# Performance work log

Hardware: AMD Instinct MI355X
Metric: run time of the kernel (lower is better)

Reference implementation:

```python
import jax, jax.numpy as jnp
import numpy as np

ALPHA = 0.01  # ELU slope from init kwargs


def setup_inputs() -> dict:
    key = jax.random.key(0)
    k1, k2, k3, k4, k5 = jax.random.split(key, 5)
    B, L, D_IN, D_ATT = 8, 2048, 256, 128
    context = jax.random.normal(k1, (B, L, D_IN), dtype=jnp.float32)
    query = jax.random.normal(k2, (B, L, D_IN), dtype=jnp.float32)
    query_mask = jax.random.randint(k3, (B, L), 0, 2, dtype=jnp.int32)
    # Linear(in_size, attention_size, bias=False) weights (stored as [in, out])
    W_in = jax.random.normal(k4, (D_IN, D_ATT), dtype=jnp.float32) * 0.05
    W_mem = jax.random.normal(k5, (D_IN, D_ATT), dtype=jnp.float32) * 0.05
    return {"context": context, "query": query, "W_in": W_in,
            "W_mem": W_mem, "query_mask": query_mask}


def reference(context, query, W_in, W_mem, query_mask):
    # VariationalDropout is identity at inference; Linear -> ELU(alpha=0.01)
    inp = jax.nn.elu(jnp.einsum('bld,df->blf', context, W_in), ALPHA)   # [B, Lc, Datt]
    mem = jax.nn.elu(jnp.einsum('bld,df->blf', query, W_mem), ALPHA)    # [B, Lq, Datt]
    scale = inp.shape[-1] ** 0.5
    logits = jnp.einsum('bcf,bqf->bcq', inp, mem) / scale               # [B, Lc, Lq]
    big = jnp.finfo(logits.dtype).max
    # mask_diag=True: kill diagonal (self) positions
    Lq = logits.shape[-1]
    eye = jnp.eye(Lq, dtype=bool)
    logits = jnp.where(eye[None, :, :], -big, logits)
    # masked_softmax over the query axis using query_mask [B, Lq]
    valid = (query_mask > 0)[:, None, :]                                # [B, 1, Lq]
    logits = jnp.where(valid, logits, -big)
    score = jax.nn.softmax(logits, axis=-1)                             # [B, Lc, Lq]
    return jnp.einsum('bcq,bqd->bcd', score, query)                     # [B, Lc, D_in]
```

## Files before the change

### kernel.cpp

```cpp
#include <hip/hip_runtime.h>
#include <math.h>

typedef short v4s __attribute__((ext_vector_type(4)));
typedef short v8s __attribute__((ext_vector_type(8)));
typedef float v4f __attribute__((ext_vector_type(4)));

#define L2E 1.4426950408889634f
#define INV_SCALE 0.08838834764831845f
#define SCL2 (INV_SCALE * L2E)

static __device__ __forceinline__ short f2bf(float x) {
    union { float f; unsigned u; } c; c.f = x;
    unsigned u = c.u;
    unsigned r = (u + 0x7fffu + ((u >> 16) & 1u)) >> 16;
    return (short)r;
}

typedef __attribute__((address_space(3))) void lds_vt;
typedef __attribute__((address_space(1))) const void gl_vt;
static __device__ __forceinline__ void gload_lds16(const void* g, void* l) {
    __builtin_amdgcn_global_load_lds((gl_vt*)g, (lds_vt*)l, 16, 0, 0);
}

__global__ __launch_bounds__(256) void k_pre(const float* __restrict__ ctx,
                                             const float* __restrict__ qry,
                                             const float* __restrict__ Win,
                                             const float* __restrict__ Wmem,
                                             const int* __restrict__ qmask,
                                             short* __restrict__ Qa,
                                             short* __restrict__ Ka,
                                             short* __restrict__ VaT,
                                             float* __restrict__ maskadd) {
    __shared__ __align__(16) char sbuf[64 * 264 * 2];
    int x = blockIdx.x;
    int tid = threadIdx.x;
    if (x < 1024) {
        short* WtS = (short*)sbuf;
        int msel = x & 255, isel = (x >> 8) & 1, nh = (x >> 9) & 1;
        const float* X = isel ? qry : ctx;
        const float* W = isel ? Wmem : Win;
        short* Y = isel ? Ka : Qa;
#pragma unroll 8
        for (int i = 0; i < 64; ++i) {
            int id = i * 256 + tid;
            int k = id >> 6, fp = id & 63;
            WtS[fp * 264 + k] = f2bf(W[k * 128 + nh * 64 + fp]);
        }
        __syncthreads();

        int w = tid >> 6, lane = tid & 63;
        int ln = lane & 15, qd = lane >> 4;
        int m0 = msel * 64 + w * 16;
        v4f zero = {0.f, 0.f, 0.f, 0.f};
        v4f o[4];
#pragma unroll
        for (int i = 0; i < 4; ++i) o[i] = zero;
#pragma unroll
        for (int kk = 0; kk < 8; ++kk) {
            const float* xp = X + (size_t)(m0 + ln) * 256 + kk * 32 + qd * 8;
            float4 x0 = *(const float4*)xp;
            float4 x1 = *(const float4*)(xp + 4);
            v8s a;
            a[0] = f2bf(x0.x); a[1] = f2bf(x0.y); a[2] = f2bf(x0.z); a[3] = f2bf(x0.w);
            a[4] = f2bf(x1.x); a[5] = f2bf(x1.y); a[6] = f2bf(x1.z); a[7] = f2bf(x1.w);
#pragma unroll
            for (int nt = 0; nt < 4; ++nt) {
                v8s bfr = *(const v8s*)(WtS + (nt * 16 + ln) * 264 + kk * 32 + qd * 8);
                o[nt] = __builtin_amdgcn_mfma_f32_16x16x32_bf16(a, bfr, o[nt], 0, 0, 0);
            }
        }
#pragma unroll
        for (int nt = 0; nt < 4; ++nt) {
#pragma unroll
            for (int r = 0; r < 4; ++r) {
                float v = o[nt][r];
                v = v > 0.f ? v : 0.01f * (__expf(v) - 1.f);
                Y[(size_t)(m0 + qd * 4 + r) * 128 + (nh * 4 + nt) * 16 + ln] = f2bf(v);
            }
        }
    } else {
        float (*tile)[65] = (float(*)[65])sbuf;
        int t = x - 1024;
        int q0 = (t & 31) * 64, d0 = ((t >> 5) & 3) * 64, b = t >> 7;
        int c = tid & 63;
        int r4 = tid >> 6;
#pragma unroll
        for (int i = 0; i < 16; ++i) {
            int r = r4 + i * 4;
            tile[r][c] = qry[(size_t)(b * 2048 + q0 + r) * 256 + d0 + c];
        }
        __syncthreads();
        int g = c >> 3, j = c & 7;
#pragma unroll
        for (int i = 0; i < 16; ++i) {
            int d = r4 + i * 4;
            int cs = ((g ^ (d & 7)) << 3) | j;
            VaT[(size_t)(b * 256 + d0 + d) * 2048 + q0 + cs] = f2bf(tile[c][d]);
        }
        if (d0 == 0 && tid < 64) {
            int qq = b * 2048 + q0 + tid;
            maskadd[qq] = (qmask[qq] > 0) ? 0.f : -__builtin_inff();
        }
    }
}

template<int NSPLIT, bool DIRECT>
__global__ __launch_bounds__(256, 2) void k_attn(const short* __restrict__ Qa,
                                                 const short* __restrict__ Ka,
                                                 const short* __restrict__ VaT,
                                                 const float* __restrict__ maskadd,
                                                 float* __restrict__ Opart,
                                                 float* __restrict__ lpart,
                                                 float* __restrict__ out) {
    __shared__ __align__(16) short VaS[2][256 * 64];
    __shared__ __align__(16) short PS[64 * 72];
    __shared__ float lS[4 * 64];

    const int STEPS = 32 / NSPLIT;
    int blk = blockIdx.x;
    int b = blk & 7;
    int t = blk >> 3;
    int c0 = (t & 31) * 64;
    int sp = t >> 5;
    int kv0 = sp * (2048 / NSPLIT);

    int tid = threadIdx.x;
    int w = tid >> 6, lane = tid & 63, ln = lane & 15, qd = lane >> 4;

    const short* qbase = Qa + (size_t)(b * 2048) * 128;
    const short* kbase = Ka + (size_t)(b * 2048 + kv0 + w * 16 + ln) * 128 + qd * 8;
    const short* vbase = VaT + (size_t)(b * 256) * 2048;
    const float* mbase = maskadd + b * 2048 + kv0 + w * 16 + qd * 4;

    v8s qf[4][4];
#pragma unroll
    for (int ct = 0; ct < 4; ++ct) {
        const short* qp = qbase + (size_t)(c0 + ct * 16 + ln) * 128 + qd * 8;
#pragma unroll
        for (int kk = 0; kk < 4; ++kk) qf[ct][kk] = *(const v8s*)(qp + kk * 32);
    }

    v4f zero = {0.f, 0.f, 0.f, 0.f};
    v4f o[4][4];
#pragma unroll
    for (int i = 0; i < 4; ++i)
#pragma unroll
        for (int j = 0; j < 4; ++j) o[i][j] = zero;
    float lacc[4] = {0.f, 0.f, 0.f, 0.f};

    auto stageV = [&](int q0s, int buf) {
        short* base = &VaS[buf][0] + w * 4096;
#pragma unroll
        for (int j = 0; j < 8; ++j) {
            int U = (w * 8 + j) * 64 + lane;
            int d = U >> 3, cc = U & 7;
            gload_lds16(vbase + (size_t)d * 2048 + q0s + cc * 8,
                        base + j * 512);
        }
    };

    stageV(kv0, 0);

    for (int it = 0; it < STEPS; ++it) {
        int q0 = kv0 + it * 64;
        int pb = it & 1;
        stageV(kv0 + ((it + 1) & (STEPS - 1)) * 64, pb ^ 1);

        v8s kf[4];
        const short* kp = kbase + (size_t)it * (64 * 128);
#pragma unroll
        for (int kk = 0; kk < 4; ++kk) kf[kk] = *(const v8s*)(kp + kk * 32);

        float4 mk = *(const float4*)(mbase + it * 64);
        int kvb = q0 + w * 16 + qd * 4;
#pragma unroll
        for (int ct = 0; ct < 4; ++ct) {
            v4f s = zero;
#pragma unroll
            for (int kk = 0; kk < 4; ++kk)
                s = __builtin_amdgcn_mfma_f32_16x16x32_bf16(kf[kk], qf[ct][kk], s, 0, 0, 0);
            int cg = c0 + ct * 16 + ln;
            v4s pw;
            float ls = 0.f;
#pragma unroll
            for (int r = 0; r < 4; ++r) {
                float v = s[r] * SCL2 + (&mk.x)[r];
                if (kvb + r == cg) v = -__builtin_inff();
                float p = exp2f(v);
                ls += p;
                pw[r] = f2bf(p);
            }
            lacc[ct] += ls;
            *(v4s*)(PS + (ct * 16 + ln) * 72 + w * 16 + qd * 4) = pw;
        }
        __syncthreads();

        const short* vs = &VaS[pb][0];
#pragma unroll
        for (int kk2 = 0; kk2 < 2; ++kk2) {
            v8s pf[4], vf[4];
#pragma unroll
            for (int ct = 0; ct < 4; ++ct)
                pf[ct] = *(const v8s*)(PS + (ct * 16 + ln) * 72 + kk2 * 32 + qd * 8);
#pragma unroll
            for (int dt = 0; dt < 4; ++dt) {
                int d = w * 64 + dt * 16 + ln;
                vf[dt] = *(const v8s*)(vs + d * 64 + (((kk2 * 4 + qd) ^ (ln & 7)) << 3));
            }
#pragma unroll
            for (int ct = 0; ct < 4; ++ct)
#pragma unroll
                for (int dt = 0; dt < 4; ++dt)
                    o[ct][dt] = __builtin_amdgcn_mfma_f32_16x16x32_bf16(pf[ct], vf[dt], o[ct][dt], 0, 0, 0);
        }
        __syncthreads();
    }

#pragma unroll
    for (int ct = 0; ct < 4; ++ct) {
        float v = lacc[ct];
        v += __shfl_xor(v, 16);
        v += __shfl_xor(v, 32);
        if (qd == 0) lS[w * 64 + ct * 16 + ln] = v;
    }
    __syncthreads();

#pragma unroll
    for (int ct = 0; ct < 4; ++ct) {
        float4 l0 = *(const float4*)(lS + 0 * 64 + ct * 16 + qd * 4);
        float4 l1 = *(const float4*)(lS + 1 * 64 + ct * 16 + qd * 4);
        float4 l2 = *(const float4*)(lS + 2 * 64 + ct * 16 + qd * 4);
        float4 l3 = *(const float4*)(lS + 3 * 64 + ct * 16 + qd * 4);
        float lv[4];
#pragma unroll
        for (int r = 0; r < 4; ++r)
            lv[r] = (&l0.x)[r] + (&l1.x)[r] + (&l2.x)[r] + (&l3.x)[r];
        int rowg = b * 2048 + c0 + ct * 16 + qd * 4;
        if (DIRECT) {
#pragma unroll
            for (int r = 0; r < 4; ++r) {
                float inv = 1.f / lv[r];
#pragma unroll
                for (int dt = 0; dt < 4; ++dt)
                    out[(size_t)(rowg + r) * 256 + w * 64 + dt * 16 + ln] = o[ct][dt][r] * inv;
            }
        } else {
            float* op = Opart + (size_t)sp * (16384 * 256);
#pragma unroll
            for (int r = 0; r < 4; ++r)
#pragma unroll
                for (int dt = 0; dt < 4; ++dt)
                    op[(size_t)(rowg + r) * 256 + w * 64 + dt * 16 + ln] = o[ct][dt][r];
            if (ln == 0)
                *(float4*)(lpart + sp * 16384 + rowg) = make_float4(lv[0], lv[1], lv[2], lv[3]);
        }
    }
}

template<int NSPLIT>
__global__ __launch_bounds__(256) void k_combine(const float* __restrict__ Opart,
                                                 const float* __restrict__ lpart,
                                                 float* __restrict__ out) {
    int idx = blockIdx.x * 256 + threadIdx.x;
    int row = idx >> 6, d4 = (idx & 63) * 4;
    float L = 0.f;
    float4 acc = {0.f, 0.f, 0.f, 0.f};
#pragma unroll
    for (int s = 0; s < NSPLIT; ++s) {
        L += lpart[s * 16384 + row];
        float4 v = *(const float4*)(Opart + (size_t)s * (16384 * 256) + (size_t)row * 256 + d4);
        acc.x += v.x; acc.y += v.y; acc.z += v.z; acc.w += v.w;
    }
    float inv = 1.f / L;
    float4 res = {acc.x * inv, acc.y * inv, acc.z * inv, acc.w * inv};
    *(float4*)(out + (size_t)row * 256 + d4) = res;
}

extern "C" void kernel_launch(void* const* d_in, const int* in_sizes, int n_in,
                              void* d_out, int out_size, void* d_ws, size_t ws_size,
                              hipStream_t stream) {
    const float* ctx  = (const float*)d_in[0];
    const float* qry  = (const float*)d_in[1];
    const float* win  = (const float*)d_in[2];
    const float* wmem = (const float*)d_in[3];
    const int* qmask  = (const int*)d_in[4];
    float* out = (float*)d_out;

    char* ws = (char*)d_ws;
    short* Qa      = (short*)(ws);
    short* Ka      = (short*)(ws + (4u << 20));
    short* VaT     = (short*)(ws + (8u << 20));
    float* maskadd = (float*)(ws + (16u << 20));
    float* lpart   = (float*)(ws + (16u << 20) + 131072);
    float* Opart   = (float*)(ws + (18u << 20));

    k_pre<<<dim3(2048), 256, 0, stream>>>(ctx, qry, win, wmem, qmask,
                                          Qa, Ka, VaT, maskadd);

    const size_t base = 18u << 20, part = 16u << 20;
    if (ws_size >= base + 2 * part) {
        k_attn<2, false><<<dim3(512), 256, 0, stream>>>(Qa, Ka, VaT, maskadd, Opart, lpart, out);
        k_combine<2><<<dim3(4096), 256, 0, stream>>>(Opart, lpart, out);
    } else {
        k_attn<1, true><<<dim3(256), 256, 0, stream>>>(Qa, Ka, VaT, maskadd, Opart, lpart, out);
    }
}
```

Before: 147.7 us.

## Replace KV split-and-combine with 32-row context tiles and software-pipelined attention loop

The attention kernel no longer splits the key range in two with a separate combine kernel. It now uses 512 blocks of 32 context rows, each covering the full key range and writing normalized output directly. The loop is unrolled by two with double-buffered K/mask register prefetch, a double-buffered swizzled P tile in LDS, manual waitcnt/barrier instead of two __syncthreads, and raised priority around the PV MFMAs. This removes the partial-output round trip through global memory and the extra launch. In exchange, each block reads all of V and K for half as many rows, doubling K/V traffic per output row. The hand-set vmcnt value is fragile if the load count changes.

```diff
diff --git a/kernel.cpp b/kernel.cpp
--- a/kernel.cpp
+++ b/kernel.cpp
@@ -104,49 +104,42 @@
     }
 }
 
-template<int NSPLIT, bool DIRECT>
 __global__ __launch_bounds__(256, 2) void k_attn(const short* __restrict__ Qa,
                                                  const short* __restrict__ Ka,
                                                  const short* __restrict__ VaT,
                                                  const float* __restrict__ maskadd,
-                                                 float* __restrict__ Opart,
-                                                 float* __restrict__ lpart,
                                                  float* __restrict__ out) {
     __shared__ __align__(16) short VaS[2][256 * 64];
-    __shared__ __align__(16) short PS[64 * 72];
-    __shared__ float lS[4 * 64];
-
-    const int STEPS = 32 / NSPLIT;
+    __shared__ __align__(16) short PSb[2][32 * 64];
+
+    const int STEPS = 32;
     int blk = blockIdx.x;
     int b = blk & 7;
-    int t = blk >> 3;
-    int c0 = (t & 31) * 64;
-    int sp = t >> 5;
-    int kv0 = sp * (2048 / NSPLIT);
+    int c0 = (blk >> 3) * 32;
 
     int tid = threadIdx.x;
     int w = tid >> 6, lane = tid & 63, ln = lane & 15, qd = lane >> 4;
 
     const short* qbase = Qa + (size_t)(b * 2048) * 128;
-    const short* kbase = Ka + (size_t)(b * 2048 + kv0 + w * 16 + ln) * 128 + qd * 8;
+    const short* kbase = Ka + (size_t)(b * 2048 + w * 16 + ln) * 128 + qd * 8;
     const short* vbase = VaT + (size_t)(b * 256) * 2048;
-    const float* mbase = maskadd + b * 2048 + kv0 + w * 16 + qd * 4;
-
-    v8s qf[4][4];
-#pragma unroll
-    for (int ct = 0; ct < 4; ++ct) {
+    const float* mbase = maskadd + b * 2048 + w * 16 + qd * 4;
+
+    v8s qf[2][4];
+#pragma unroll
+    for (int ct = 0; ct < 2; ++ct) {
         const short* qp = qbase + (size_t)(c0 + ct * 16 + ln) * 128 + qd * 8;
 #pragma unroll
         for (int kk = 0; kk < 4; ++kk) qf[ct][kk] = *(const v8s*)(qp + kk * 32);
     }
 
     v4f zero = {0.f, 0.f, 0.f, 0.f};
-    v4f o[4][4];
-#pragma unroll
-    for (int i = 0; i < 4; ++i)
+    v4f o[2][4];
+#pragma unroll
+    for (int i = 0; i < 2; ++i)
 #pragma unroll
         for (int j = 0; j < 4; ++j) o[i][j] = zero;
-    float lacc[4] = {0.f, 0.f, 0.f, 0.f};
+    float lacc[2] = {0.f, 0.f};
 
     auto stageV = [&](int q0s, int buf) {
         short* base = &VaS[buf][0] + w * 4096;
@@ -159,121 +152,113 @@
         }
     };
 
-    stageV(kv0, 0);
-
-    for (int it = 0; it < STEPS; ++it) {
-        int q0 = kv0 + it * 64;
-        int pb = it & 1;
-        stageV(kv0 + ((it + 1) & (STEPS - 1)) * 64, pb ^ 1);
-
-        v8s kf[4];
-        const short* kp = kbase + (size_t)it * (64 * 128);
-#pragma unroll
-        for (int kk = 0; kk < 4; ++kk) kf[kk] = *(const v8s*)(kp + kk * 32);
-
-        float4 mk = *(const float4*)(mbase + it * 64);
-        int kvb = q0 + w * 16 + qd * 4;
-#pragma unroll
-        for (int ct = 0; ct < 4; ++ct) {
-            v4f s = zero;
-#pragma unroll
-            for (int kk = 0; kk < 4; ++kk)
-                s = __builtin_amdgcn_mfma_f32_16x16x32_bf16(kf[kk], qf[ct][kk], s, 0, 0, 0);
-            int cg = c0 + ct * 16 + ln;
-            v4s pw;
-            float ls = 0.f;
-#pragma unroll
-            for (int r = 0; r < 4; ++r) {
-                float v = s[r] * SCL2 + (&mk.x)[r];
-                if (kvb + r == cg) v = -__builtin_inff();
-                float p = exp2f(v);
-                ls += p;
-                pw[r] = f2bf(p);
-            }
-            lacc[ct] += ls;
-            *(v4s*)(PS + (ct * 16 + ln) * 72 + w * 16 + qd * 4) = pw;
-        }
-        __syncthreads();
-
-        const short* vs = &VaS[pb][0];
-#pragma unroll
-        for (int kk2 = 0; kk2 < 2; ++kk2) {
-            v8s pf[4], vf[4];
-#pragma unroll
-            for (int ct = 0; ct < 4; ++ct)
-                pf[ct] = *(const v8s*)(PS + (ct * 16 + ln) * 72 + kk2 * 32 + qd * 8);
-#pragma unroll
-            for (int dt = 0; dt < 4; ++dt) {
-                int d = w * 64 + dt * 16 + ln;
-                vf[dt] = *(const v8s*)(vs + d * 64 + (((kk2 * 4 + qd) ^ (ln & 7)) << 3));
-            }
-#pragma unroll
-            for (int ct = 0; ct < 4; ++ct)
-#pragma unroll
-                for (int dt = 0; dt < 4; ++dt)
-                    o[ct][dt] = __builtin_amdgcn_mfma_f32_16x16x32_bf16(pf[ct], vf[dt], o[ct][dt], 0, 0, 0);
-        }
-        __syncthreads();
-    }
-
-#pragma unroll
-    for (int ct = 0; ct < 4; ++ct) {
+    stageV(0, 0);
+    v8s kfA[4], kfB[4];
+    float4 mkA, mkB;
+#pragma unroll
+    for (int kk = 0; kk < 4; ++kk) kfA[kk] = *(const v8s*)(kbase + kk * 32);
+    mkA = *(const float4*)(mbase);
+
+#define ATT_STEP(IT, KFC, MKC, KFN, MKN) do {                                  \
+    int q0 = (IT) * 64;                                                        \
+    int pb = (IT) & 1;                                                         \
+    int itn = ((IT) + 1) & (STEPS - 1);                                        \
+    stageV(itn * 64, pb ^ 1);                                                  \
+    {                                                                          \
+        const short* kp = kbase + (size_t)itn * 8192;                          \
+        _Pragma("unroll")                                                      \
+        for (int kk = 0; kk < 4; ++kk) KFN[kk] = *(const v8s*)(kp + kk * 32);  \
+        MKN = *(const float4*)(mbase + itn * 64);                              \
+    }                                                                          \
+      \
+    asm volatile("s_waitcnt vmcnt(13)" ::: "memory");                          \
+    short* PScur = &PSb[pb][0];                                                \
+    int kvb = q0 + w * 16 + qd * 4;                                            \
+    _Pragma("unroll")                                                          \
+    for (int ct = 0; ct < 2; ++ct) {                                           \
+        v4f s = zero;                                                          \
+        _Pragma("unroll")                                                      \
+        for (int kk = 0; kk < 4; ++kk)                                         \
+            s = __builtin_amdgcn_mfma_f32_16x16x32_bf16(KFC[kk], qf[ct][kk],   \
+                                                        s, 0, 0, 0);           \
+        int cg = c0 + ct * 16 + ln;                                            \
+        v4s pw;                                                                \
+        float ls = 0.f;                                                        \
+        _Pragma("unroll")                                                      \
+        for (int r = 0; r < 4; ++r) {                                          \
+            float v = s[r] * SCL2 + (&MKC.x)[r];                               \
+            if (kvb + r == cg) v = -__builtin_inff();                          \
+            float p = exp2f(v);                                                \
+            ls += p;                                                           \
+            pw[r] = f2bf(p);                                                   \
+        }                                                                      \
+        lacc[ct] += ls;                                                        \
+        int hs = ((w * 2 + (qd >> 1)) ^ (ln & 7));                             \
+        *(v4s*)(PScur + (ct * 16 + ln) * 64 + hs * 8 + (qd & 1) * 4) = pw;     \
+    }                                                                          \
+    asm volatile("s_waitcnt lgkmcnt(0)" ::: "memory");                         \
+    __builtin_amdgcn_s_barrier();                                              \
+    asm volatile("" ::: "memory");                                             \
+    const short* vs = &VaS[pb][0];                                             \
+    __builtin_amdgcn_s_setprio(1);                                             \
+    _Pragma("unroll")                                                          \
+    for (int kk2 = 0; kk2 < 2; ++kk2) {                                        \
+        v8s pf[2], vf[4];                                                      \
+        _Pragma("unroll")                                                      \
+        for (int ct = 0; ct < 2; ++ct)                                         \
+            pf[ct] = *(const v8s*)(PScur + (ct * 16 + ln) * 64 +               \
+                                   (((kk2 * 4 + qd) ^ (ln & 7)) << 3));        \
+        _Pragma("unroll")                                                      \
+        for (int dt = 0; dt < 4; ++dt) {                                       \
+            int d = w * 64 + dt * 16 + ln;                                     \
+            vf[dt] = *(const v8s*)(vs + d * 64 +                               \
+                                   (((kk2 * 4 + qd) ^ (ln & 7)) << 3));        \
+        }                                                                      \
+        _Pragma("unroll")                                                      \
+        for (int ct = 0; ct < 2; ++ct)                                         \
+            _Pragma("unroll")                                                  \
+            for (int dt = 0; dt < 4; ++dt)                                     \
+                o[ct][dt] = __builtin_amdgcn_mfma_f32_16x16x32_bf16(           \
+                    pf[ct], vf[dt], o[ct][dt], 0, 0, 0);                       \
+    }                                                                          \
+    __builtin_amdgcn_s_setprio(0);                                             \
+} while (0)
+
+#pragma unroll 1
+    for (int it2 = 0; it2 < STEPS; it2 += 2) {
+        ATT_STEP(it2, kfA, mkA, kfB, mkB);
+        ATT_STEP(it2 + 1, kfB, mkB, kfA, mkA);
+    }
+#undef ATT_STEP
+
+    __syncthreads();
+    float* lS = (float*)&PSb[0][0];
+#pragma unroll
+    for (int ct = 0; ct < 2; ++ct) {
         float v = lacc[ct];
         v += __shfl_xor(v, 16);
         v += __shfl_xor(v, 32);
-        if (qd == 0) lS[w * 64 + ct * 16 + ln] = v;
+        if (qd == 0) lS[w * 32 + ct * 16 + ln] = v;
     }
     __syncthreads();
 
 #pragma unroll
-    for (int ct = 0; ct < 4; ++ct) {
-        float4 l0 = *(const float4*)(lS + 0 * 64 + ct * 16 + qd * 4);
-        float4 l1 = *(const float4*)(lS + 1 * 64 + ct * 16 + qd * 4);
-        float4 l2 = *(const float4*)(lS + 2 * 64 + ct * 16 + qd * 4);
-        float4 l3 = *(const float4*)(lS + 3 * 64 + ct * 16 + qd * 4);
-        float lv[4];
-#pragma unroll
-        for (int r = 0; r < 4; ++r)
-            lv[r] = (&l0.x)[r] + (&l1.x)[r] + (&l2.x)[r] + (&l3.x)[r];
+    for (int ct = 0; ct < 2; ++ct) {
+        float4 l0 = *(const float4*)(lS + 0 * 32 + ct * 16 + qd * 4);
+        float4 l1 = *(const float4*)(lS + 1 * 32 + ct * 16 + qd * 4);
+        float4 l2 = *(const float4*)(lS + 2 * 32 + ct * 16 + qd * 4);
+        float4 l3 = *(const float4*)(lS + 3 * 32 + ct * 16 + qd * 4);
         int rowg = b * 2048 + c0 + ct * 16 + qd * 4;
-        if (DIRECT) {
-#pragma unroll
-            for (int r = 0; r < 4; ++r) {
-                float inv = 1.f / lv[r];
-#pragma unroll
-                for (int dt = 0; dt < 4; ++dt)
-                    out[(size_t)(rowg + r) * 256 + w * 64 + dt * 16 + ln] = o[ct][dt][r] * inv;
-            }
-        } else {
-            float* op = Opart + (size_t)sp * (16384 * 256);
-#pragma unroll
-            for (int r = 0; r < 4; ++r)
-#pragma unroll
-                for (int dt = 0; dt < 4; ++dt)
-                    op[(size_t)(rowg + r) * 256 + w * 64 + dt * 16 + ln] = o[ct][dt][r];
-            if (ln == 0)
-                *(float4*)(lpart + sp * 16384 + rowg) = make_float4(lv[0], lv[1], lv[2], lv[3]);
-        }
-    }
-}
-
-template<int NSPLIT>
-__global__ __launch_bounds__(256) void k_combine(const float* __restrict__ Opart,
-                                                 const float* __restrict__ lpart,
-                                                 float* __restrict__ out) {
-    int idx = blockIdx.x * 256 + threadIdx.x;
-    int row = idx >> 6, d4 = (idx & 63) * 4;
-    float L = 0.f;
-    float4 acc = {0.f, 0.f, 0.f, 0.f};
-#pragma unroll
-    for (int s = 0; s < NSPLIT; ++s) {
-        L += lpart[s * 16384 + row];
-        float4 v = *(const float4*)(Opart + (size_t)s * (16384 * 256) + (size_t)row * 256 + d4);
-        acc.x += v.x; acc.y += v.y; acc.z += v.z; acc.w += v.w;
-    }
-    float inv = 1.f / L;
-    float4 res = {acc.x * inv, acc.y * inv, acc.z * inv, acc.w * inv};
-    *(float4*)(out + (size_t)row * 256 + d4) = res;
+#pragma unroll
+        for (int r = 0; r < 4; ++r) {
+            float lv = (&l0.x)[r] + (&l1.x)[r] + (&l2.x)[r] + (&l3.x)[r];
+            float inv = 1.f / lv;
+#pragma unroll
+            for (int dt = 0; dt < 4; ++dt)
+                out[(size_t)(rowg + r) * 256 + w * 64 + dt * 16 + ln] =
+                    o[ct][dt][r] * inv;
+        }
+    }
 }
 
 extern "C" void kernel_launch(void* const* d_in, const int* in_sizes, int n_in,
@@ -291,17 +276,8 @@
     short* Ka      = (short*)(ws + (4u << 20));
     short* VaT     = (short*)(ws + (8u << 20));
     float* maskadd = (float*)(ws + (16u << 20));
-    float* lpart   = (float*)(ws + (16u << 20) + 131072);
-    float* Opart   = (float*)(ws + (18u << 20));
 
     k_pre<<<dim3(2048), 256, 0, stream>>>(ctx, qry, win, wmem, qmask,
                                           Qa, Ka, VaT, maskadd);
-
-    const size_t base = 18u << 20, part = 16u << 20;
-    if (ws_size >= base + 2 * part) {
-        k_attn<2, false><<<dim3(512), 256, 0, stream>>>(Qa, Ka, VaT, maskadd, Opart, lpart, out);
-        k_combine<2><<<dim3(4096), 256, 0, stream>>>(Opart, lpart, out);
-    } else {
-        k_attn<1, true><<<dim3(256), 256, 0, stream>>>(Qa, Ka, VaT, maskadd, Opart, lpart, out);
-    }
-}
+    k_attn<<<dim3(512), 256, 0, stream>>>(Qa, Ka, VaT, maskadd, out);
+}
```

Result: slower. 152.9 us (+3.5%).
